# Performance work log

Hardware: AMD Instinct MI355X
Metric: run time of the kernel (lower is better)

The kernel has to match this reference:

```python
import jax, jax.numpy as jnp
import numpy as np

N = 50000      # nodes
E = 800000     # edges (before self loops)
IN = 128       # in_channels
HID = 64       # hidden_channels
HEADS = 4      # num_heads
OUT = 40       # out_channels
NEG_SLOPE = 0.2


def setup_inputs() -> dict:
    key = jax.random.key(0)
    ks = jax.random.split(key, 16)
    x = jax.random.normal(ks[0], (N, IN), dtype=jnp.float32)
    edge_index = jax.random.randint(ks[1], (2, E), 0, N, dtype=jnp.int64)

    def lin(k, fan_in, fan_out):
        return jax.random.normal(k, (fan_in, fan_out), dtype=jnp.float32) * (1.0 / np.sqrt(fan_in))

    def att(k, h, c):
        return jax.random.normal(k, (h, c), dtype=jnp.float32) * (1.0 / np.sqrt(c))

    return {
        "x": x, "edge_index": edge_index,
        "W1": lin(ks[2], IN, HEADS * HID),
        "as1": att(ks[3], HEADS, HID), "ad1": att(ks[4], HEADS, HID),
        "b1": jnp.zeros((HEADS * HID,), jnp.float32),
        "W2": lin(ks[5], HEADS * HID, HEADS * HID),
        "as2": att(ks[6], HEADS, HID), "ad2": att(ks[7], HEADS, HID),
        "b2": jnp.zeros((HEADS * HID,), jnp.float32),
        "W3": lin(ks[8], HEADS * HID, OUT),
        "as3": att(ks[9], 1, OUT), "ad3": att(ks[10], 1, OUT),
        "b3": jnp.zeros((OUT,), jnp.float32),
    }


def _gat_layer(x, src, dst, W, a_src, a_dst, b):
    """One GATConv: linear -> per-edge attention -> segment softmax -> scatter-sum."""
    n = x.shape[0]
    H, C = a_src.shape
    h = (x @ W).reshape(n, H, C)                       # [N,H,C]
    al_s = jnp.einsum('nhc,hc->nh', h, a_src)          # [N,H]
    al_d = jnp.einsum('nhc,hc->nh', h, a_dst)          # [N,H]
    alpha = jax.nn.leaky_relu(al_s[src] + al_d[dst], NEG_SLOPE)  # [Etot,H]
    m = jax.ops.segment_max(alpha, dst, num_segments=n)          # stable softmax over incoming edges
    e = jnp.exp(alpha - m[dst])
    denom = jax.ops.segment_sum(e, dst, num_segments=n)
    attn = e / denom[dst]                              # [Etot,H]
    out = jax.ops.segment_sum(h[src] * attn[:, :, None], dst, num_segments=n)  # [N,H,C]
    return out.reshape(n, H * C) + b


def reference(x, edge_index, W1, as1, ad1, b1, W2, as2, ad2, b2, W3, as3, ad3, b3):
    # add self loops once (PyG GATConv default add_self_loops=True)
    loops = jnp.arange(N, dtype=edge_index.dtype)
    src = jnp.concatenate([edge_index[0], loops])
    dst = jnp.concatenate([edge_index[1], loops])

    h = _gat_layer(x, src, dst, W1, as1, ad1, b1)
    h = jax.nn.relu(h)                                 # dropout is identity in eval mode
    h = _gat_layer(h, src, dst, W2, as2, ad2, b2)
    h = jax.nn.relu(h)
    h = _gat_layer(h, src, dst, W3, as3, ad3, b3)      # final layer: 1 head
    return jax.nn.log_softmax(h, axis=-1)
```

## Files before the change

kernel.cpp:

```cpp
#include <hip/hip_runtime.h>
#include <math.h>

#define N_NODES 50000
#define N_EDGES 800000
#define ETOT    (N_EDGES + N_NODES)
#define EPAD_MAX 1200000
#define IN_CH   128
#define OUT_CH  40
#define NEG     0.2f
#define CAP     64

#define P1   32
#define NPC  1563
#define CCAP 34000
#define P2   16
#define NPF  98
#define NFINE (P1 * P2)
#define FCAP 2400

typedef __attribute__((ext_vector_type(8))) short bf16x8;
typedef __attribute__((ext_vector_type(4))) float f32x4;
typedef __attribute__((ext_vector_type(2))) float f32x2;

__device__ inline unsigned short f2bf(float f) {
    unsigned int u = __float_as_uint(f);
    return (unsigned short)((u + 0x7FFFu + ((u >> 16) & 1u)) >> 16);
}
__device__ inline float bf2f(unsigned short u) {
    return __uint_as_float((unsigned int)u << 16);
}
__device__ inline float lrelu(float a) { return (a > 0.f) ? a : NEG * a; }

__global__ __launch_bounds__(256) void k_b1(const int* __restrict__ ei,
                                            int* __restrict__ ccur,
                                            unsigned int* __restrict__ cbuf) {
    __shared__ int lcnt[P1], lbase[P1], lcur[P1];
    int tid = threadIdx.x;
    if (tid < P1) lcnt[tid] = 0;
    __syncthreads();
    for (int i = blockIdx.x * 256 + tid; i < ETOT; i += 256 * 256) {
        int d = (i < N_EDGES) ? ei[N_EDGES + i] : (i - N_EDGES);
        atomicAdd(&lcnt[d / NPC], 1);
    }
    __syncthreads();
    if (tid < P1) {
        lbase[tid] = atomicAdd(&ccur[tid], lcnt[tid]);
        lcur[tid] = 0;
    }
    __syncthreads();
    for (int i = blockIdx.x * 256 + tid; i < ETOT; i += 256 * 256) {
        int s, d;
        if (i < N_EDGES) { s = ei[i]; d = ei[N_EDGES + i]; }
        else             { s = i - N_EDGES; d = s; }
        int p = d / NPC;
        int off = atomicAdd(&lcur[p], 1);
        cbuf[(long)p * CCAP + lbase[p] + off] = (unsigned int)s | ((unsigned int)d << 16);
    }
}

__global__ __launch_bounds__(256) void k_b2(const int* __restrict__ ccur,
                                            const unsigned int* __restrict__ cbuf,
                                            int* __restrict__ fcur,
                                            unsigned int* __restrict__ fbuf) {
    __shared__ int lcnt[P2], lbase[P2], lcur2[P2];
    int c = blockIdx.x >> 3;
    int sub = blockIdx.x & 7;
    int tid = threadIdx.x;
    int n = ccur[c];
    if (tid < P2) lcnt[tid] = 0;
    __syncthreads();
    int base = c * NPC;
    for (int i = sub * 256 + tid; i < n; i += 8 * 256) {
        int d = (int)(cbuf[(long)c * CCAP + i] >> 16);
        atomicAdd(&lcnt[(d - base) / NPF], 1);
    }
    __syncthreads();
    if (tid < P2) {
        lbase[tid] = atomicAdd(&fcur[c * P2 + tid], lcnt[tid]);
        lcur2[tid] = 0;
    }
    __syncthreads();
    for (int i = sub * 256 + tid; i < n; i += 8 * 256) {
        unsigned int u = cbuf[(long)c * CCAP + i];
        int d = (int)(u >> 16);
        int j = (d - base) / NPF;
        int off = atomicAdd(&lcur2[j], 1);
        fbuf[(long)(c * P2 + j) * FCAP + lbase[j] + off] = u;
    }
}

__global__ __launch_bounds__(256) void k_deg(const int* __restrict__ fcur,
                                             const unsigned int* __restrict__ fbuf,
                                             int* __restrict__ deg) {
    __shared__ int cnt[NPF];
    int f = blockIdx.x;
    int tid = threadIdx.x;
    int c = f >> 4, j = f & 15;
    int n0 = c * NPC + j * NPF;
    int nend = min(min(n0 + NPF, (c + 1) * NPC), N_NODES);
    if (tid < NPF) cnt[tid] = 0;
    __syncthreads();
    int n = fcur[f];
    for (int i = tid; i < n; i += 256)
        atomicAdd(&cnt[(int)(fbuf[(long)f * FCAP + i] >> 16) - n0], 1);
    __syncthreads();
    if (tid < NPF && n0 + tid < nend) deg[n0 + tid] = cnt[tid];
}

__global__ void k_scan1(const int* __restrict__ deg, int* __restrict__ start,
                        int* __restrict__ bsum) {
    __shared__ int sh[256];
    int tid = threadIdx.x;
    int i = blockIdx.x * 256 + tid;
    int v = (i < N_NODES) ? ((deg[i] + 7) & ~7) : 0;
    int x = v;
    sh[tid] = x;
    __syncthreads();
    #pragma unroll
    for (int off = 1; off < 256; off <<= 1) {
        int t = (tid >= off) ? sh[tid - off] : 0;
        __syncthreads();
        x += t;
        sh[tid] = x;
        __syncthreads();
    }
    if (i < N_NODES) start[i] = x - v;
    if (tid == 255) bsum[blockIdx.x] = x;
}

__global__ void k_scan3(int* __restrict__ start, const int* __restrict__ bsum,
                        int nb) {
    __shared__ int sh[256];
    __shared__ int ex[256];
    int tid = threadIdx.x;
    int v = (tid < nb) ? bsum[tid] : 0;
    int x = v;
    sh[tid] = x;
    __syncthreads();
    #pragma unroll
    for (int off = 1; off < 256; off <<= 1) {
        int t = (tid >= off) ? sh[tid - off] : 0;
        __syncthreads();
        x += t;
        sh[tid] = x;
        __syncthreads();
    }
    ex[tid] = x - v;
    __syncthreads();
    int add = ex[blockIdx.x];
    int i = blockIdx.x * 256 + tid;
    if (i < N_NODES) start[i] += add;
}

__global__ __launch_bounds__(256) void k_scat(const int* __restrict__ fcur,
                                              const unsigned int* __restrict__ fbuf,
                                              const int* __restrict__ start,
                                              int* __restrict__ eSrc) {
    __shared__ int offs[NPF];
    __shared__ int base[NPF];
    int f = blockIdx.x;
    int tid = threadIdx.x;
    int c = f >> 4, j = f & 15;
    int n0 = c * NPC + j * NPF;
    int nend = min(min(n0 + NPF, (c + 1) * NPC), N_NODES);
    int nn = nend - n0;
    if (tid < NPF && tid < nn) {
        int b = start[n0 + tid];
        offs[tid] = b;
        base[tid] = b;
    }
    __syncthreads();
    int n = fcur[f];
    for (int i = tid; i < n; i += 256) {
        unsigned int u = fbuf[(long)f * FCAP + i];
        int d = (int)(u >> 16);
        int pos = atomicAdd(&offs[d - n0], 1);
        eSrc[pos] = (int)(u & 0xFFFFu);
    }
    __syncthreads();
    if (tid < NPF && tid < nn) {
        int endp = offs[tid];
        int dg = endp - base[tid];
        int stop = base[tid] + ((dg + 7) & ~7);
        for (int k2 = endp; k2 < stop; ++k2) eSrc[k2] = -1;
    }
}

__global__ void k_wt_all(const float* __restrict__ W1, const float* __restrict__ W2,
                         const float* __restrict__ W3,
                         unsigned short* __restrict__ Wt1,
                         unsigned short* __restrict__ Wt2,
                         unsigned short* __restrict__ Wt3) {
    int i = blockIdx.x * blockDim.x + threadIdx.x;
    if (i < 32768) {
        int n = i >> 7, k = i & 127;
        Wt1[i] = f2bf(W1[(long)k * 256 + n]);
    } else if (i < 98304) {
        int j = i - 32768;
        int n = j >> 8, k = j & 255;
        Wt2[j] = f2bf(W2[(long)k * 256 + n]);
    } else if (i < 114688) {
        int j = i - 98304;
        int n = j >> 8, k = j & 255;
        Wt3[j] = (n < OUT_CH) ? f2bf(W3[(long)k * OUT_CH + n]) : (unsigned short)0;
    }
}

#define PITCH 40
template<int BN, int FM, int FN, bool CVT, bool FP8OUT, bool L4>
__global__ __launch_bounds__(256) void k_mfma(const void* __restrict__ Araw,
                                              const unsigned short* __restrict__ Bt,
                                              void* __restrict__ Cout,
                                              const float* __restrict__ a_s,
                                              const float* __restrict__ a_d,
                                              float* __restrict__ als,
                                              float* __restrict__ ald,
                                              int M, int K, int Ncol) {
    __shared__ unsigned short As[128 * PITCH];
    __shared__ unsigned short Bs[BN * PITCH];
    const int WCOLS = BN / (FN * 16);
    int tid = threadIdx.x;
    int wave = tid >> 6, lane = tid & 63;
    int quad = lane >> 4, l16 = lane & 15;
    int wr = wave / WCOLS, wc = wave % WCOLS;
    long row0 = (long)blockIdx.x * 128;
    int col0 = blockIdx.y * BN;

    f32x4 acc[FM][FN] = {};

    for (int k0 = 0; k0 < K; k0 += 32) {
        for (int c = tid; c < 512; c += 256) {
            int r = c >> 2, kp = (c & 3) << 3;
            long gr = row0 + r;
            if (CVT) {
                const float* A32 = (const float*)Araw;
                ushort4 lo = {0,0,0,0}, hi = {0,0,0,0};
                if (gr < M) {
                    float4 v0 = *(const float4*)(A32 + gr * K + k0 + kp);
                    float4 v1 = *(const float4*)(A32 + gr * K + k0 + kp + 4);
                    lo.x = f2bf(v0.x); lo.y = f2bf(v0.y); lo.z = f2bf(v0.z); lo.w = f2bf(v0.w);
                    hi.x = f2bf(v1.x); hi.y = f2bf(v1.y); hi.z = f2bf(v1.z); hi.w = f2bf(v1.w);
                }
                *(ushort4*)(As + r * PITCH + kp) = lo;
                *(ushort4*)(As + r * PITCH + kp + 4) = hi;
            } else {
                const unsigned short* A16 = (const unsigned short*)Araw;
                uint4 v = {0u, 0u, 0u, 0u};
                if (gr < M) v = *(const uint4*)(A16 + gr * K + k0 + kp);
                *(uint4*)(As + r * PITCH + kp) = v;
            }
        }
        for (int c = tid; c < BN * 4; c += 256) {
            int r = c >> 2, kp = (c & 3) << 3;
            uint4 v = *(const uint4*)(Bt + (long)(col0 + r) * K + k0 + kp);
            *(uint4*)(Bs + r * PITCH + kp) = v;
        }
        __syncthreads();
        bf16x8 af[FM], bfr[FN];
        #pragma unroll
        for (int i = 0; i < FM; ++i)
            af[i] = *(const bf16x8*)(As + (wr * FM * 16 + i * 16 + l16) * PITCH + quad * 8);
        #pragma unroll
        for (int j = 0; j < FN; ++j)
            bfr[j] = *(const bf16x8*)(Bs + (wc * FN * 16 + j * 16 + l16) * PITCH + quad * 8);
        #pragma unroll
        for (int i = 0; i < FM; ++i)
            #pragma unroll
            for (int j = 0; j < FN; ++j)
                acc[i][j] = __builtin_amdgcn_mfma_f32_16x16x32_bf16(af[i], bfr[j], acc[i][j], 0, 0, 0);
        __syncthreads();
    }

    {
        int head = L4 ? (blockIdx.y * WCOLS + wc) : 0;
        float as_v[FN], ad_v[FN];
        #pragma unroll
        for (int j = 0; j < FN; ++j) {
            int cidx = j * 16 + l16;
            if (L4) {
                as_v[j] = a_s[head * 64 + cidx];
                ad_v[j] = a_d[head * 64 + cidx];
            } else {
                as_v[j] = (cidx < OUT_CH) ? a_s[cidx] : 0.f;
                ad_v[j] = (cidx < OUT_CH) ? a_d[cidx] : 0.f;
            }
        }
        #pragma unroll
        for (int i = 0; i < FM; ++i) {
            #pragma unroll
            for (int v = 0; v < 4; ++v) {
                float ps = acc[i][0][v] * as_v[0] + acc[i][1][v] * as_v[1]
                         + acc[i][2][v] * as_v[2] + acc[i][3][v] * as_v[3];
                float pd = acc[i][0][v] * ad_v[0] + acc[i][1][v] * ad_v[1]
                         + acc[i][2][v] * ad_v[2] + acc[i][3][v] * ad_v[3];
                #pragma unroll
                for (int off = 1; off < 16; off <<= 1) {
                    ps += __shfl_xor(ps, off);
                    pd += __shfl_xor(pd, off);
                }
                if (l16 == 0) {
                    long row = row0 + wr * (FM * 16) + i * 16 + quad * 4 + v;
                    if (row < M) {
                        if (L4) { als[row * 4 + head] = ps; ald[row * 4 + head] = pd; }
                        else    { als[row] = ps; ald[row] = pd; }
                    }
                }
            }
        }
    }

    if (FP8OUT) {
        unsigned char* C8 = (unsigned char*)Cout;
        #pragma unroll
        for (int i = 0; i < FM; ++i) {
            #pragma unroll
            for (int v = 0; v < 4; ++v) {
                long row = row0 + wr * FM * 16 + i * 16 + quad * 4 + v;
                if (row < M) {
                    int p01 = __builtin_amdgcn_cvt_pk_fp8_f32(acc[i][0][v], acc[i][1][v], 0, false);
                    int p23 = __builtin_amdgcn_cvt_pk_fp8_f32(acc[i][2][v], acc[i][3][v], 0, false);
                    unsigned char* b = C8 + row * 256 + col0 + wc * (FN * 16) + l16;
                    b[0]  = (unsigned char)(p01 & 0xFF);
                    b[16] = (unsigned char)((p01 >> 8) & 0xFF);
                    b[32] = (unsigned char)(p23 & 0xFF);
                    b[48] = (unsigned char)((p23 >> 8) & 0xFF);
                }
            }
        }
    } else {
        unsigned short* C = (unsigned short*)Cout;
        #pragma unroll
        for (int i = 0; i < FM; ++i) {
            long rowb = row0 + wr * FM * 16 + i * 16 + quad * 4;
            #pragma unroll
            for (int j = 0; j < FN; ++j) {
                int col = col0 + wc * FN * 16 + j * 16 + l16;
                if (col < Ncol) {
                    #pragma unroll
                    for (int v = 0; v < 4; ++v) {
                        long r = rowb + v;
                        if (r < M) C[r * Ncol + col] = f2bf(acc[i][j][v]);
                    }
                }
            }
        }
    }
}

__global__ __launch_bounds__(256) void k_agg4(const unsigned char* __restrict__ h8,
                                              const int* __restrict__ start,
                                              const int* __restrict__ deg,
                                              const int* __restrict__ eSrc,
                                              const float* __restrict__ als,
                                              const float* __restrict__ ald,
                                              const float* __restrict__ bias,
                                              unsigned short* __restrict__ out) {
    __shared__ float wbuf[4][CAP * 4];
    __shared__ int   sbuf[4][CAP];
    int wid = threadIdx.x >> 6;
    int node = (blockIdx.x * blockDim.x + threadIdx.x) >> 6;
    int lane = threadIdx.x & 63;
    if (node >= N_NODES) return;
    int st = start[node];
    int dgp = (deg[node] + 7) & ~7;
    const int* ep = eSrc + st;

    int l16 = lane & 15, headw = lane >> 4;
    float aldd4 = ald[node * 4 + headw];
    int ncap = (dgp < CAP) ? dgp : CAP;
    for (int c = 0; c < ncap; c += 16) {
        int slot = c + l16;
        bool ok = (slot < ncap);
        int raw = ok ? ep[slot] : -1;
        int ss = (raw < 0) ? 0 : raw;
        float a = als[(long)ss * 4 + headw] + aldd4;
        float w = (raw < 0) ? 0.f : __expf(lrelu(a));
        if (ok) {
            wbuf[wid][slot * 4 + headw] = w;
            if (headw == 0) sbuf[wid][slot] = ss;
        }
    }

    int half = lane >> 5;
    int hl = lane & 31;
    int head8 = hl >> 3;
    float den = 0.f;
    f32x2 acc2[4] = {};

    int ncpair = ncap >> 1;
    int jA = 0, jB = ncpair - 4;

    auto do_pairs = [&](int p0, int p1, int p2, int p3) {
        int slot[4] = {p0 * 2 + half, p1 * 2 + half, p2 * 2 + half, p3 * 2 + half};
        int s[4];
        float w[4];
        #pragma unroll
        for (int u = 0; u < 4; ++u) {
            s[u] = sbuf[wid][slot[u]];
            w[u] = wbuf[wid][slot[u] * 4 + head8];
        }
        uint2 hv[4];
        #pragma unroll
        for (int u = 0; u < 4; ++u)
            hv[u] = *(const uint2*)(h8 + (long)s[u] * 256 + hl * 8);
        #pragma unroll
        for (int u = 0; u < 4; ++u) {
            den += w[u];
            f32x2 w2; w2.x = w[u]; w2.y = w[u];
            acc2[0] += w2 * __builtin_amdgcn_cvt_pk_f32_fp8((int)hv[u].x, false);
            acc2[1] += w2 * __builtin_amdgcn_cvt_pk_f32_fp8((int)hv[u].x, true);
            acc2[2] += w2 * __builtin_amdgcn_cvt_pk_f32_fp8((int)hv[u].y, false);
            acc2[3] += w2 * __builtin_amdgcn_cvt_pk_f32_fp8((int)hv[u].y, true);
        }
    };

    while (jA < jB) {
        do_pairs(jA, jA + 1, jB, jB + 1);
        do_pairs(jA + 2, jA + 3, jB + 2, jB + 3);
        jA += 4; jB -= 4;
    }
    if (jA == jB) {
        do_pairs(jA, jA + 1, jA + 2, jA + 3);
    }

    if (dgp > ncap) {
        float aldd8 = ald[node * 4 + head8];
        for (int j = ncap; j < dgp; j += 2) {
            int raw = ep[j + half];
            int ss = (raw < 0) ? 0 : raw;
            float w = (raw < 0) ? 0.f : __expf(lrelu(als[(long)ss * 4 + head8] + aldd8));
            uint2 hv = *(const uint2*)(h8 + (long)ss * 256 + hl * 8);
            den += w;
            f32x2 w2; w2.x = w; w2.y = w;
            acc2[0] += w2 * __builtin_amdgcn_cvt_pk_f32_fp8((int)hv.x, false);
            acc2[1] += w2 * __builtin_amdgcn_cvt_pk_f32_fp8((int)hv.x, true);
            acc2[2] += w2 * __builtin_amdgcn_cvt_pk_f32_fp8((int)hv.y, false);
            acc2[3] += w2 * __builtin_amdgcn_cvt_pk_f32_fp8((int)hv.y, true);
        }
    }

    den += __shfl_xor(den, 32);
    #pragma unroll
    for (int c = 0; c < 4; ++c) {
        acc2[c].x += __shfl_xor(acc2[c].x, 32);
        acc2[c].y += __shfl_xor(acc2[c].y, 32);
    }

    if (half == 0) {
        float inv = 1.f / den;
        int cb = hl * 8;
        float4 b0 = *(const float4*)(bias + cb);
        float4 b1 = *(const float4*)(bias + cb + 4);
        float v0 = fmaxf(acc2[0].x * inv + b0.x, 0.f);
        float v1 = fmaxf(acc2[0].y * inv + b0.y, 0.f);
        float v2 = fmaxf(acc2[1].x * inv + b0.z, 0.f);
        float v3 = fmaxf(acc2[1].y * inv + b0.w, 0.f);
        float v4 = fmaxf(acc2[2].x * inv + b1.x, 0.f);
        float v5 = fmaxf(acc2[2].y * inv + b1.y, 0.f);
        float v6 = fmaxf(acc2[3].x * inv + b1.z, 0.f);
        float v7 = fmaxf(acc2[3].y * inv + b1.w, 0.f);
        uint4 o;
        o.x = (unsigned int)f2bf(v0) | ((unsigned int)f2bf(v1) << 16);
        o.y = (unsigned int)f2bf(v2) | ((unsigned int)f2bf(v3) << 16);
        o.z = (unsigned int)f2bf(v4) | ((unsigned int)f2bf(v5) << 16);
        o.w = (unsigned int)f2bf(v6) | ((unsigned int)f2bf(v7) << 16);
        *(uint4*)(out + (long)node * 256 + cb) = o;
    }
}

__global__ __launch_bounds__(256) void k_agg1(const unsigned short* __restrict__ h,
                                              const int* __restrict__ start,
                                              const int* __restrict__ deg,
                                              const int* __restrict__ eSrc,
                                              const float* __restrict__ als,
                                              const float* __restrict__ ald,
                                              const float* __restrict__ bias,
                                              float* __restrict__ out) {
    int node = (blockIdx.x * blockDim.x + threadIdx.x) >> 6;
    int lane = threadIdx.x & 63;
    if (node >= N_NODES) return;
    int q = lane >> 4, r = lane & 15;
    bool act = (r < 10);
    int st = start[node];
    int dgp = (deg[node] + 7) & ~7;
    const int* ep = eSrc + st;
    float aldd = ald[node];

    float den = 0.f;
    float4 acc = {0.f, 0.f, 0.f, 0.f};

    int j = 0;
    for (; j + 16 <= dgp; j += 16) {
        int base = j + q * 4;
        int s[4];
        float w[4];
        #pragma unroll
        for (int u = 0; u < 4; ++u) s[u] = ep[base + u];
        #pragma unroll
        for (int u = 0; u < 4; ++u) {
            int raw = s[u];
            int ss = (raw < 0) ? 0 : raw;
            w[u] = (raw < 0) ? 0.f : __expf(lrelu(als[ss] + aldd));
            s[u] = ss;
        }
        ushort4 hh[4];
        #pragma unroll
        for (int u = 0; u < 4; ++u) {
            ushort4 t = {0, 0, 0, 0};
            if (act) t = *(const ushort4*)(h + (long)s[u] * OUT_CH + r * 4);
            hh[u] = t;
        }
        #pragma unroll
        for (int u = 0; u < 4; ++u) {
            den += w[u];
            acc.x += w[u] * bf2f(hh[u].x);
            acc.y += w[u] * bf2f(hh[u].y);
            acc.z += w[u] * bf2f(hh[u].z);
            acc.w += w[u] * bf2f(hh[u].w);
        }
    }
    if (j < dgp) {
        int base = j + q * 2;
        int s[2];
        float w[2];
        #pragma unroll
        for (int u = 0; u < 2; ++u) s[u] = ep[base + u];
        #pragma unroll
        for (int u = 0; u < 2; ++u) {
            int raw = s[u];
            int ss = (raw < 0) ? 0 : raw;
            w[u] = (raw < 0) ? 0.f : __expf(lrelu(als[ss] + aldd));
            s[u] = ss;
        }
        ushort4 hh[2];
        #pragma unroll
        for (int u = 0; u < 2; ++u) {
            ushort4 t = {0, 0, 0, 0};
            if (act) t = *(const ushort4*)(h + (long)s[u] * OUT_CH + r * 4);
            hh[u] = t;
        }
        #pragma unroll
        for (int u = 0; u < 2; ++u) {
            den += w[u];
            acc.x += w[u] * bf2f(hh[u].x);
            acc.y += w[u] * bf2f(hh[u].y);
            acc.z += w[u] * bf2f(hh[u].z);
            acc.w += w[u] * bf2f(hh[u].w);
        }
    }

    #pragma unroll
    for (int off = 16; off < 64; off <<= 1) {
        acc.x += __shfl_xor(acc.x, off);
        acc.y += __shfl_xor(acc.y, off);
        acc.z += __shfl_xor(acc.z, off);
        acc.w += __shfl_xor(acc.w, off);
        den   += __shfl_xor(den, off);
    }
    float inv = 1.f / den;
    float4 bv = {0.f, 0.f, 0.f, 0.f};
    if (act) bv = *(const float4*)(bias + r * 4);
    float4 v;
    v.x = acc.x * inv + bv.x;
    v.y = acc.y * inv + bv.y;
    v.z = acc.z * inv + bv.z;
    v.w = acc.w * inv + bv.w;
    float mx = act ? fmaxf(fmaxf(v.x, v.y), fmaxf(v.z, v.w)) : -INFINITY;
    #pragma unroll
    for (int off = 1; off < 16; off <<= 1) mx = fmaxf(mx, __shfl_xor(mx, off));
    float sum = act ? (__expf(v.x - mx) + __expf(v.y - mx) + __expf(v.z - mx) + __expf(v.w - mx)) : 0.f;
    #pragma unroll
    for (int off = 1; off < 16; off <<= 1) sum += __shfl_xor(sum, off);
    float lse = mx + logf(sum);
    if (q == 0 && act) {
        float4 o;
        o.x = v.x - lse;
        o.y = v.y - lse;
        o.z = v.z - lse;
        o.w = v.w - lse;
        *(float4*)(out + (long)node * OUT_CH + r * 4) = o;
    }
}

extern "C" void kernel_launch(void* const* d_in, const int* in_sizes, int n_in,
                              void* d_out, int out_size, void* d_ws, size_t ws_size,
                              hipStream_t stream) {
    (void)in_sizes; (void)n_in; (void)out_size; (void)ws_size;
    const float* x   = (const float*)d_in[0];
    const int*   ei  = (const int*)d_in[1];
    const float* W1  = (const float*)d_in[2];
    const float* as1 = (const float*)d_in[3];
    const float* ad1 = (const float*)d_in[4];
    const float* b1  = (const float*)d_in[5];
    const float* W2  = (const float*)d_in[6];
    const float* as2 = (const float*)d_in[7];
    const float* ad2 = (const float*)d_in[8];
    const float* b2  = (const float*)d_in[9];
    const float* W3  = (const float*)d_in[10];
    const float* as3 = (const float*)d_in[11];
    const float* ad3 = (const float*)d_in[12];
    const float* b3  = (const float*)d_in[13];
    float* out = (float*)d_out;

    char* p = (char*)d_ws;
    auto alloc = [&](size_t b) { char* r = p; p += (b + 255) & ~(size_t)255; return r; };
    int*   deg   = (int*)alloc((size_t)N_NODES * 4);
    int*   start = (int*)alloc((size_t)N_NODES * 4);
    int*   bsum  = (int*)alloc(256 * 4);
    int*   cnts  = (int*)alloc((size_t)(P1 + NFINE) * 4);
    unsigned int* cbuf = (unsigned int*)alloc((size_t)P1 * CCAP * 4);
    unsigned int* fbuf = (unsigned int*)alloc((size_t)NFINE * FCAP * 4);
    int*   eSrc  = (int*)alloc((size_t)EPAD_MAX * 4);
    float* als   = (float*)alloc((size_t)N_NODES * 4 * 4);
    float* ald   = (float*)alloc((size_t)N_NODES * 4 * 4);
    unsigned char*  hA8  = (unsigned char*)alloc((size_t)N_NODES * 256);
    unsigned short* hBbf = (unsigned short*)alloc((size_t)N_NODES * 256 * 2);
    unsigned short* h3bf = (unsigned short*)alloc((size_t)N_NODES * OUT_CH * 2);
    unsigned short* Wt1  = (unsigned short*)alloc((size_t)256 * IN_CH * 2);
    unsigned short* Wt2  = (unsigned short*)alloc((size_t)256 * 256 * 2);
    unsigned short* Wt3  = (unsigned short*)alloc((size_t)64 * 256 * 2);
    int* ccur = cnts;
    int* fcur = cnts + P1;

    const int NB = (N_NODES + 255) / 256;
    const int WB = (N_NODES + 3) / 4;
    const int MB = (N_NODES + 127) / 128;

    hipMemsetAsync(cnts, 0, (size_t)(P1 + NFINE) * 4, stream);
    k_b1<<<256, 256, 0, stream>>>(ei, ccur, cbuf);
    k_b2<<<256, 256, 0, stream>>>(ccur, cbuf, fcur, fbuf);
    k_deg<<<NFINE, 256, 0, stream>>>(fcur, fbuf, deg);
    k_scan1<<<NB, 256, 0, stream>>>(deg, start, bsum);
    k_scan3<<<NB, 256, 0, stream>>>(start, bsum, NB);
    k_scat<<<NFINE, 256, 0, stream>>>(fcur, fbuf, start, eSrc);

    k_wt_all<<<448, 256, 0, stream>>>(W1, W2, W3, Wt1, Wt2, Wt3);

    k_mfma<128, 4, 4, true, true, true><<<dim3(MB, 2), 256, 0, stream>>>(
        x, Wt1, hA8, as1, ad1, als, ald, N_NODES, IN_CH, 256);
    k_agg4<<<WB, 256, 0, stream>>>(hA8, start, deg, eSrc, als, ald, b1, hBbf);

    k_mfma<128, 4, 4, false, true, true><<<dim3(MB, 2), 256, 0, stream>>>(
        hBbf, Wt2, hA8, as2, ad2, als, ald, N_NODES, 256, 256);
    k_agg4<<<WB, 256, 0, stream>>>(hA8, start, deg, eSrc, als, ald, b2, hBbf);

    k_mfma<64, 2, 4, false, false, false><<<dim3(MB, 1), 256, 0, stream>>>(
        hBbf, Wt3, h3bf, as3, ad3, als, ald, N_NODES, 256, OUT_CH);
    k_agg1<<<WB, 256, 0, stream>>>(h3bf, start, deg, eSrc, als, ald, b3, out);
}
```

Before: 321.0 us.

## Single-pass edge bucketing, fuse weight prep, split aggregation across two waves

```diff
diff --git a/kernel.cpp b/kernel.cpp
--- a/kernel.cpp
+++ b/kernel.cpp
@@ -10,13 +10,9 @@
 #define NEG     0.2f
 #define CAP     64
 
-#define P1   32
-#define NPC  1563
-#define CCAP 34000
-#define P2   16
-#define NPF  98
-#define NFINE (P1 * P2)
-#define FCAP 2400
+#define NPF   98
+#define NFINE 512
+#define FCAP  2400
 
 typedef __attribute__((ext_vector_type(8))) short bf16x8;
 typedef __attribute__((ext_vector_type(4))) float f32x4;
@@ -31,61 +27,52 @@
 }
 __device__ inline float lrelu(float a) { return (a > 0.f) ? a : NEG * a; }
 
-__global__ __launch_bounds__(256) void k_b1(const int* __restrict__ ei,
-                                            int* __restrict__ ccur,
-                                            unsigned int* __restrict__ cbuf) {
-    __shared__ int lcnt[P1], lbase[P1], lcur[P1];
+__global__ __launch_bounds__(256) void k_bkt(const int* __restrict__ ei,
+                                             int* __restrict__ fcur,
+                                             unsigned int* __restrict__ fbuf,
+                                             const float* __restrict__ W1,
+                                             const float* __restrict__ W2,
+                                             const float* __restrict__ W3,
+                                             unsigned short* __restrict__ Wt1,
+                                             unsigned short* __restrict__ Wt2,
+                                             unsigned short* __restrict__ Wt3) {
+    if (blockIdx.x >= 256) {
+        int i = (blockIdx.x - 256) * 256 + threadIdx.x;
+        if (i < 32768) {
+            int n = i >> 7, k = i & 127;
+            Wt1[i] = f2bf(W1[(long)k * 256 + n]);
+        } else if (i < 98304) {
+            int j = i - 32768;
+            int n = j >> 8, k = j & 255;
+            Wt2[j] = f2bf(W2[(long)k * 256 + n]);
+        } else if (i < 114688) {
+            int j = i - 98304;
+            int n = j >> 8, k = j & 255;
+            Wt3[j] = (n < OUT_CH) ? f2bf(W3[(long)k * OUT_CH + n]) : (unsigned short)0;
+        }
+        return;
+    }
+    __shared__ int lcnt[NFINE], lbase[NFINE], lcur[NFINE];
     int tid = threadIdx.x;
-    if (tid < P1) lcnt[tid] = 0;
+    for (int i = tid; i < NFINE; i += 256) lcnt[i] = 0;
     __syncthreads();
     for (int i = blockIdx.x * 256 + tid; i < ETOT; i += 256 * 256) {
         int d = (i < N_EDGES) ? ei[N_EDGES + i] : (i - N_EDGES);
-        atomicAdd(&lcnt[d / NPC], 1);
-    }
-    __syncthreads();
-    if (tid < P1) {
-        lbase[tid] = atomicAdd(&ccur[tid], lcnt[tid]);
-        lcur[tid] = 0;
+        atomicAdd(&lcnt[d / NPF], 1);
+    }
+    __syncthreads();
+    for (int i = tid; i < NFINE; i += 256) {
+        lbase[i] = atomicAdd(&fcur[i], lcnt[i]);
+        lcur[i] = 0;
     }
     __syncthreads();
     for (int i = blockIdx.x * 256 + tid; i < ETOT; i += 256 * 256) {
         int s, d;
         if (i < N_EDGES) { s = ei[i]; d = ei[N_EDGES + i]; }
         else             { s = i - N_EDGES; d = s; }
-        int p = d / NPC;
+        int p = d / NPF;
         int off = atomicAdd(&lcur[p], 1);
-        cbuf[(long)p * CCAP + lbase[p] + off] = (unsigned int)s | ((unsigned int)d << 16);
-    }
-}
-
-__global__ __launch_bounds__(256) void k_b2(const int* __restrict__ ccur,
-                                            const unsigned int* __restrict__ cbuf,
-                                            int* __restrict__ fcur,
-                                            unsigned int* __restrict__ fbuf) {
-    __shared__ int lcnt[P2], lbase[P2], lcur2[P2];
-    int c = blockIdx.x >> 3;
-    int sub = blockIdx.x & 7;
-    int tid = threadIdx.x;
-    int n = ccur[c];
-    if (tid < P2) lcnt[tid] = 0;
-    __syncthreads();
-    int base = c * NPC;
-    for (int i = sub * 256 + tid; i < n; i += 8 * 256) {
-        int d = (int)(cbuf[(long)c * CCAP + i] >> 16);
-        atomicAdd(&lcnt[(d - base) / NPF], 1);
-    }
-    __syncthreads();
-    if (tid < P2) {
-        lbase[tid] = atomicAdd(&fcur[c * P2 + tid], lcnt[tid]);
-        lcur2[tid] = 0;
-    }
-    __syncthreads();
-    for (int i = sub * 256 + tid; i < n; i += 8 * 256) {
-        unsigned int u = cbuf[(long)c * CCAP + i];
-        int d = (int)(u >> 16);
-        int j = (d - base) / NPF;
-        int off = atomicAdd(&lcur2[j], 1);
-        fbuf[(long)(c * P2 + j) * FCAP + lbase[j] + off] = u;
+        fbuf[(long)p * FCAP + lbase[p] + off] = (unsigned int)s | ((unsigned int)d << 16);
     }
 }
 
@@ -95,9 +82,8 @@
     __shared__ int cnt[NPF];
     int f = blockIdx.x;
     int tid = threadIdx.x;
-    int c = f >> 4, j = f & 15;
-    int n0 = c * NPC + j * NPF;
-    int nend = min(min(n0 + NPF, (c + 1) * NPC), N_NODES);
+    int n0 = f * NPF;
+    int nend = min(n0 + NPF, N_NODES);
     if (tid < NPF) cnt[tid] = 0;
     __syncthreads();
     int n = fcur[f];
@@ -160,9 +146,8 @@
     __shared__ int base[NPF];
     int f = blockIdx.x;
     int tid = threadIdx.x;
-    int c = f >> 4, j = f & 15;
-    int n0 = c * NPC + j * NPF;
-    int nend = min(min(n0 + NPF, (c + 1) * NPC), N_NODES);
+    int n0 = f * NPF;
+    int nend = min(n0 + NPF, N_NODES);
     int nn = nend - n0;
     if (tid < NPF && tid < nn) {
         int b = start[n0 + tid];
@@ -183,26 +168,6 @@
         int dg = endp - base[tid];
         int stop = base[tid] + ((dg + 7) & ~7);
         for (int k2 = endp; k2 < stop; ++k2) eSrc[k2] = -1;
-    }
-}
-
-__global__ void k_wt_all(const float* __restrict__ W1, const float* __restrict__ W2,
-                         const float* __restrict__ W3,
-                         unsigned short* __restrict__ Wt1,
-                         unsigned short* __restrict__ Wt2,
-                         unsigned short* __restrict__ Wt3) {
-    int i = blockIdx.x * blockDim.x + threadIdx.x;
-    if (i < 32768) {
-        int n = i >> 7, k = i & 127;
-        Wt1[i] = f2bf(W1[(long)k * 256 + n]);
-    } else if (i < 98304) {
-        int j = i - 32768;
-        int n = j >> 8, k = j & 255;
-        Wt2[j] = f2bf(W2[(long)k * 256 + n]);
-    } else if (i < 114688) {
-        int j = i - 98304;
-        int n = j >> 8, k = j & 255;
-        Wt3[j] = (n < OUT_CH) ? f2bf(W3[(long)k * OUT_CH + n]) : (unsigned short)0;
     }
 }
 
@@ -355,29 +320,37 @@
                                               const float* __restrict__ ald,
                                               const float* __restrict__ bias,
                                               unsigned short* __restrict__ out) {
-    __shared__ float wbuf[4][CAP * 4];
-    __shared__ int   sbuf[4][CAP];
-    int wid = threadIdx.x >> 6;
-    int node = (blockIdx.x * blockDim.x + threadIdx.x) >> 6;
-    int lane = threadIdx.x & 63;
-    if (node >= N_NODES) return;
+    __shared__ float wbuf[2][CAP * 4];
+    __shared__ int   sbuf[2][CAP];
+    __shared__ float red[2][32][9];
+    int tid = threadIdx.x;
+    int wave = tid >> 6;
+    int nib = wave >> 1;
+    int sub = wave & 1;
+    int node = blockIdx.x * 2 + nib;
+    int lane = tid & 63;
+
     int st = start[node];
     int dgp = (deg[node] + 7) & ~7;
     const int* ep = eSrc + st;
+    int ncap = (dgp < CAP) ? dgp : CAP;
+    int hc = ((ncap >> 1) + 7) & ~7;
+    if (hc > ncap) hc = ncap;
+    int lo = sub ? hc : 0;
+    int hi = sub ? ncap : hc;
 
     int l16 = lane & 15, headw = lane >> 4;
     float aldd4 = ald[node * 4 + headw];
-    int ncap = (dgp < CAP) ? dgp : CAP;
-    for (int c = 0; c < ncap; c += 16) {
+    for (int c = lo; c < hi; c += 16) {
         int slot = c + l16;
-        bool ok = (slot < ncap);
+        bool ok = (slot < hi);
         int raw = ok ? ep[slot] : -1;
         int ss = (raw < 0) ? 0 : raw;
         float a = als[(long)ss * 4 + headw] + aldd4;
         float w = (raw < 0) ? 0.f : __expf(lrelu(a));
         if (ok) {
-            wbuf[wid][slot * 4 + headw] = w;
-            if (headw == 0) sbuf[wid][slot] = ss;
+            wbuf[nib][slot * 4 + headw] = w;
+            if (headw == 0) sbuf[nib][slot] = ss;
         }
     }
 
@@ -387,17 +360,15 @@
     float den = 0.f;
     f32x2 acc2[4] = {};
 
-    int ncpair = ncap >> 1;
-    int jA = 0, jB = ncpair - 4;
-
-    auto do_pairs = [&](int p0, int p1, int p2, int p3) {
-        int slot[4] = {p0 * 2 + half, p1 * 2 + half, p2 * 2 + half, p3 * 2 + half};
+    int pairs = (hi - lo) >> 1;
+    for (int pi = 0; pi < pairs; pi += 4) {
         int s[4];
         float w[4];
         #pragma unroll
         for (int u = 0; u < 4; ++u) {
-            s[u] = sbuf[wid][slot[u]];
-            w[u] = wbuf[wid][slot[u] * 4 + head8];
+            int slot = lo + (pi + u) * 2 + half;
+            s[u] = sbuf[nib][slot];
+            w[u] = wbuf[nib][slot * 4 + head8];
         }
         uint2 hv[4];
         #pragma unroll
@@ -412,18 +383,9 @@
             acc2[2] += w2 * __builtin_amdgcn_cvt_pk_f32_fp8((int)hv[u].y, false);
             acc2[3] += w2 * __builtin_amdgcn_cvt_pk_f32_fp8((int)hv[u].y, true);
         }
-    };
-
-    while (jA < jB) {
-        do_pairs(jA, jA + 1, jB, jB + 1);
-        do_pairs(jA + 2, jA + 3, jB + 2, jB + 3);
-        jA += 4; jB -= 4;
-    }
-    if (jA == jB) {
-        do_pairs(jA, jA + 1, jA + 2, jA + 3);
-    }
-
-    if (dgp > ncap) {
+    }
+
+    if (sub == 1 && dgp > ncap) {
         float aldd8 = ald[node * 4 + head8];
         for (int j = ncap; j < dgp; j += 2) {
             int raw = ep[j + half];
@@ -446,7 +408,23 @@
         acc2[c].y += __shfl_xor(acc2[c].y, 32);
     }
 
-    if (half == 0) {
+    if (sub == 1 && half == 0) {
+        #pragma unroll
+        for (int c = 0; c < 4; ++c) {
+            red[nib][hl][c * 2]     = acc2[c].x;
+            red[nib][hl][c * 2 + 1] = acc2[c].y;
+        }
+        red[nib][hl][8] = den;
+    }
+    __syncthreads();
+    if (sub == 0 && half == 0) {
+        #pragma unroll
+        for (int c = 0; c < 4; ++c) {
+            acc2[c].x += red[nib][hl][c * 2];
+            acc2[c].y += red[nib][hl][c * 2 + 1];
+        }
+        den += red[nib][hl][8];
+
         float inv = 1.f / den;
         int cb = hl * 8;
         float4 b0 = *(const float4*)(bias + cb);
@@ -607,8 +585,7 @@
     int*   deg   = (int*)alloc((size_t)N_NODES * 4);
     int*   start = (int*)alloc((size_t)N_NODES * 4);
     int*   bsum  = (int*)alloc(256 * 4);
-    int*   cnts  = (int*)alloc((size_t)(P1 + NFINE) * 4);
-    unsigned int* cbuf = (unsigned int*)alloc((size_t)P1 * CCAP * 4);
+    int*   fcur  = (int*)alloc((size_t)NFINE * 4);
     unsigned int* fbuf = (unsigned int*)alloc((size_t)NFINE * FCAP * 4);
     int*   eSrc  = (int*)alloc((size_t)EPAD_MAX * 4);
     float* als   = (float*)alloc((size_t)N_NODES * 4 * 4);
@@ -619,30 +596,26 @@
     unsigned short* Wt1  = (unsigned short*)alloc((size_t)256 * IN_CH * 2);
     unsigned short* Wt2  = (unsigned short*)alloc((size_t)256 * 256 * 2);
     unsigned short* Wt3  = (unsigned short*)alloc((size_t)64 * 256 * 2);
-    int* ccur = cnts;
-    int* fcur = cnts + P1;
 
     const int NB = (N_NODES + 255) / 256;
     const int WB = (N_NODES + 3) / 4;
+    const int AB = N_NODES / 2;
     const int MB = (N_NODES + 127) / 128;
 
-    hipMemsetAsync(cnts, 0, (size_t)(P1 + NFINE) * 4, stream);
-    k_b1<<<256, 256, 0, stream>>>(ei, ccur, cbuf);
-    k_b2<<<256, 256, 0, stream>>>(ccur, cbuf, fcur, fbuf);
+    hipMemsetAsync(fcur, 0, (size_t)NFINE * 4, stream);
+    k_bkt<<<256 + 448, 256, 0, stream>>>(ei, fcur, fbuf, W1, W2, W3, Wt1, Wt2, Wt3);
     k_deg<<<NFINE, 256, 0, stream>>>(fcur, fbuf, deg);
     k_scan1<<<NB, 256, 0, stream>>>(deg, start, bsum);
     k_scan3<<<NB, 256, 0, stream>>>(start, bsum, NB);
     k_scat<<<NFINE, 256, 0, stream>>>(fcur, fbuf, start, eSrc);
 
-    k_wt_all<<<448, 256, 0, stream>>>(W1, W2, W3, Wt1, Wt2, Wt3);
-
     k_mfma<128, 4, 4, true, true, true><<<dim3(MB, 2), 256, 0, stream>>>(
         x, Wt1, hA8, as1, ad1, als, ald, N_NODES, IN_CH, 256);
-    k_agg4<<<WB, 256, 0, stream>>>(hA8, start, deg, eSrc, als, ald, b1, hBbf);
+    k_agg4<<<AB, 256, 0, stream>>>(hA8, start, deg, eSrc, als, ald, b1, hBbf);
 
     k_mfma<128, 4, 4, false, true, true><<<dim3(MB, 2), 256, 0, stream>>>(
         hBbf, Wt2, hA8, as2, ad2, als, ald, N_NODES, 256, 256);
-    k_agg4<<<WB, 256, 0, stream>>>(hA8, start, deg, eSrc, als, ald, b2, hBbf);
+    k_agg4<<<AB, 256, 0, stream>>>(hA8, start, deg, eSrc, als, ald, b2, hBbf);
 
     k_mfma<64, 2, 4, false, false, false><<<dim3(MB, 1), 256, 0, stream>>>(
         hBbf, Wt3, h3bf, as3, ad3, als, ald, N_NODES, 256, OUT_CH);
```

After: 322.0 us. No clear change (+0.3%).
